# Kernel optimization log

Measured on AMD Instinct MI355X. Metric: run time of the kernel, lower is better.

The kernel has to match this reference:

```python
import jax, jax.numpy as jnp
import numpy as np

N_Q, N_X, N_Z = 1024, 512, 512
N_PER = N_Q + N_X + N_Z        # 2048 nodes per graph
B = 16                          # graphs per batch
DEG = 16                        # avg in/out degree
E_PER = N_PER * DEG
N = B * N_PER                   # 32768 total nodes
E = B * E_PER                   # 524288 total edges
HID, HEADS, L = 128, 4, 3
DH = HID // HEADS               # 32 per-head dim
EPS = 1e-5


def setup_inputs() -> dict:
    key = jax.random.key(0)
    ks = jax.random.split(key, 10)
    # one-hot node-type features (qubit / X-stab / Z-stab), tiled over batch
    sn = jnp.zeros((N_PER, 3), jnp.float32)
    sn = sn.at[:N_Q, 0].set(1.0).at[N_Q:N_Q + N_X, 1].set(1.0).at[N_Q + N_X:, 2].set(1.0)
    x = jnp.tile(sn, (B, 1))  # [N,3]
    # random sparse edges, graph-local then offset (mimics dense_to_sparse + Batch)
    src = jax.random.randint(ks[0], (B, E_PER), 0, N_PER)
    dst = jax.random.randint(ks[1], (B, E_PER), 0, N_PER)
    off = (jnp.arange(B) * N_PER)[:, None]
    edge_src = (src + off).reshape(-1).astype(jnp.int32)
    edge_dst = (dst + off).reshape(-1).astype(jnp.int32)
    seg = jnp.repeat(jnp.arange(B, dtype=jnp.int32), N_PER)  # graph id per node
    s = 0.05
    return dict(
        x=x, edge_src=edge_src, edge_dst=edge_dst, seg=seg,
        in_w=jax.random.normal(ks[2], (3, HID)) * s, in_b=jnp.zeros((HID,)),
        qw=jax.random.normal(ks[3], (L, HID, HID)) * s, qb=jnp.zeros((L, HID)),
        kw=jax.random.normal(ks[4], (L, HID, HID)) * s, kb=jnp.zeros((L, HID)),
        vw=jax.random.normal(ks[5], (L, HID, HID)) * s, vb=jnp.zeros((L, HID)),
        sw=jax.random.normal(ks[6], (L, HID, HID)) * s, sb=jnp.zeros((L, HID)),
        fw=jax.random.normal(ks[7], (L, HID, HID)) * s, fb=jnp.zeros((L, HID)),
        ln_g=jnp.ones((L, HID)), ln_b=jnp.zeros((L, HID)),
    )


def _layer_norm(h, g, b):
    mu = jnp.mean(h, axis=-1, keepdims=True)
    var = jnp.mean(jnp.square(h - mu), axis=-1, keepdims=True)
    return (h - mu) * jax.lax.rsqrt(var + EPS) * g + b


def reference(x, edge_src, edge_dst, seg, in_w, in_b, qw, qb, kw, kb, vw, vb,
              sw, sb, fw, fb, ln_g, ln_b):
    scale = 1.0 / jnp.sqrt(jnp.float32(DH))
    h = x @ in_w + in_b  # [N,HID]
    for i in range(L):
        h_res = h
        # TransformerConv: per-edge multi-head attention (softmax over in-neighbors)
        q = (h @ qw[i] + qb[i]).reshape(N, HEADS, DH)
        k = (h @ kw[i] + kb[i]).reshape(N, HEADS, DH)
        v = (h @ vw[i] + vb[i]).reshape(N, HEADS, DH)
        logits = jnp.einsum('ehd,ehd->eh', q[edge_dst], k[edge_src]) * scale  # [E,H]
        m = jax.ops.segment_max(logits, edge_dst, num_segments=N)             # [N,H]
        e = jnp.exp(logits - m[edge_dst])
        z = jax.ops.segment_sum(e, edge_dst, num_segments=N)                  # [N,H]
        alpha = e / z[edge_dst]
        agg = jax.ops.segment_sum(alpha[:, :, None] * v[edge_src], edge_dst,
                                  num_segments=N).reshape(N, HID)
        h = agg + h @ sw[i] + sb[i]        # root/skip linear (root_weight=True)
        # dropout is a no-op in eval mode
        h = h + jax.nn.relu(h @ fw[i] + fb[i])   # FFN residual
        h = h + h_res                            # outer residual
        h = jax.nn.relu(_layer_norm(h, ln_g[i], ln_b[i]))
    # global_mean_pool over graphs
    tot = jax.ops.segment_sum(h, seg, num_segments=B)                       # [B,HID]
    cnt = jax.ops.segment_sum(jnp.ones((N, 1), h.dtype), seg, num_segments=B)
    return tot / cnt
```

## Files before the change

### kernel.cpp

```cpp
#include <hip/hip_runtime.h>
#include <hip/hip_bf16.h>

#define N_TOT 32768
#define E_TOT 524288
#define HID 128
#define B_GR 16
#define NPER 2048
#define LAYERS 3
#define EPSLN 1e-5f
#define ELLW 64
#define SCALE 0.17677669529663687f

typedef float f4 __attribute__((ext_vector_type(4)));
typedef short bf16x8 __attribute__((ext_vector_type(8)));
typedef unsigned short u16x4 __attribute__((ext_vector_type(4)));

__device__ __forceinline__ unsigned short f2bf_rne(float x) {
    unsigned u = __float_as_uint(x);
    unsigned r = (u + 0x7FFFu + ((u >> 16) & 1u)) >> 16;
    return (unsigned short)r;
}

__device__ __forceinline__ float bf2f(unsigned short u) {
    return __uint_as_float(((unsigned)u) << 16);
}

__device__ __forceinline__ void unpack8(uint4 w, float* f) {
    f[0] = __uint_as_float(w.x << 16); f[1] = __uint_as_float(w.x & 0xFFFF0000u);
    f[2] = __uint_as_float(w.y << 16); f[3] = __uint_as_float(w.y & 0xFFFF0000u);
    f[4] = __uint_as_float(w.z << 16); f[5] = __uint_as_float(w.z & 0xFFFF0000u);
    f[6] = __uint_as_float(w.w << 16); f[7] = __uint_as_float(w.w & 0xFFFF0000u);
}

__global__ __launch_bounds__(256) void k_zp(const float* __restrict__ qw, const float* __restrict__ kw,
                                            const float* __restrict__ vw, const float* __restrict__ sw,
                                            const float* __restrict__ fw, unsigned short* __restrict__ wt,
                                            int* __restrict__ cursor, float* __restrict__ outz) {
    if (blockIdx.x < 960) {
        int mid = blockIdx.x >> 6;
        int within = (blockIdx.x & 63) * 256 + threadIdx.x;
        int l = mid / 5, t = mid % 5;
        const float* src = (t == 0 ? qw : t == 1 ? kw : t == 2 ? vw : t == 3 ? sw : fw) + l * HID * HID;
        int c = within >> 7;
        int kk = within & 127;
        int k = kk ^ ((c & 7) << 3);
        float sc = (t == 0) ? SCALE : 1.0f;
        wt[mid * HID * HID + c * HID + kk] = f2bf_rne(src[k * HID + c] * sc);
    } else if (blockIdx.x < 992) {
        int i = (blockIdx.x - 960) * 256 + threadIdx.x;
        reinterpret_cast<int4*>(cursor)[i] = int4{0, 0, 0, 0};
    } else {
        f4 z4 = {0.f, 0.f, 0.f, 0.f};
        reinterpret_cast<f4*>(outz)[threadIdx.x * 2] = z4;
        reinterpret_cast<f4*>(outz)[threadIdx.x * 2 + 1] = z4;
    }
}

__global__ __launch_bounds__(256) void k_scatter_ell(const int* __restrict__ src, const int* __restrict__ dst,
                                                     int* __restrict__ cursor, unsigned short* __restrict__ ell) {
    int e = blockIdx.x * 256 + threadIdx.x;
    if (e < E_TOT) {
        int d = dst[e];
        int pos = atomicAdd(&cursor[d], 1);
        if (pos < ELLW) ell[d * ELLW + pos] = (unsigned short)src[e];
    }
}

__device__ __forceinline__ void stage_A(const float* __restrict__ A, int r0,
                                        unsigned short (*A_lds)[HID], int tid) {
    #pragma unroll
    for (int p = 0; p < 8; ++p) {
        int idx = p * 256 + tid;
        int row = idx >> 5;
        int k0 = (idx & 31) * 4;
        f4 v = reinterpret_cast<const f4*>(A + (size_t)r0 * HID)[idx];
        u16x4 b = {f2bf_rne(v.x), f2bf_rne(v.y), f2bf_rne(v.z), f2bf_rne(v.w)};
        *reinterpret_cast<u16x4*>(&A_lds[row][k0 ^ ((row & 7) << 3)]) = b;
    }
}

#define GEMM_COMPUTE(acc, AL)                                                               \
    {                                                                                       \
        _Pragma("unroll")                                                                   \
        for (int ks = 0; ks < 4; ++ks) {                                                    \
            bf16x8 a0 = *reinterpret_cast<const bf16x8*>(                                   \
                &AL[wm * 32 + lr][(ks * 32 + lg * 8) ^ swz]);                               \
            bf16x8 a1 = *reinterpret_cast<const bf16x8*>(                                   \
                &AL[wm * 32 + 16 + lr][(ks * 32 + lg * 8) ^ swz]);                          \
            _Pragma("unroll")                                                               \
            for (int n = 0; n < 4; ++n) {                                                   \
                bf16x8 b = *reinterpret_cast<const bf16x8*>(                                \
                    &W_lds[wn * 64 + n * 16 + lr][(ks * 32 + lg * 8) ^ swz]);               \
                acc[0][n] = __builtin_amdgcn_mfma_f32_16x16x32_bf16(a0, b, acc[0][n], 0, 0, 0); \
                acc[1][n] = __builtin_amdgcn_mfma_f32_16x16x32_bf16(a1, b, acc[1][n], 0, 0, 0); \
            }                                                                               \
        }                                                                                   \
    }

#define QKV_EPILOGUE(ACC, T_IDX)                                                            \
    {                                                                                       \
        _Pragma("unroll")                                                                   \
        for (int n = 0; n < 4; ++n) {                                                       \
            int col = wn * 64 + n * 16 + lr;                                                \
            float bs = biases[T_IDX][col];                                                  \
            if (T_IDX == 0) bs *= SCALE;                                                    \
            unsigned short* outp = (T_IDX == 0) ? oq : okv + ((T_IDX == 2) ? 128 : 0);      \
            const size_t stride = (T_IDX == 0) ? HID : 256;                                 \
            _Pragma("unroll")                                                               \
            for (int m = 0; m < 2; ++m) {                                                   \
                _Pragma("unroll")                                                           \
                for (int r = 0; r < 4; ++r) {                                               \
                    int row = r0 + wm * 32 + m * 16 + lg * 4 + r;                           \
                    outp[(size_t)row * stride + col] = f2bf_rne(ACC[m][n][r] + bs);         \
                }                                                                           \
            }                                                                               \
        }                                                                                   \
    }

__global__ __launch_bounds__(256) void k_init_qkv(const float* __restrict__ x,
                                                  const float* __restrict__ in_w,
                                                  const float* __restrict__ in_b,
                                                  const unsigned short* __restrict__ wl,
                                                  const float* __restrict__ qb, const float* __restrict__ kb,
                                                  const float* __restrict__ vb,
                                                  float* __restrict__ h,
                                                  unsigned short* __restrict__ oq,
                                                  unsigned short* __restrict__ okv) {
    __shared__ unsigned short A_lds[64][HID];
    __shared__ unsigned short W_lds[HID][HID];
    int tid = threadIdx.x;
    int r0 = blockIdx.x * 64;
    int lane = tid & 63, w = tid >> 6;
    int wm = w >> 1, wn = w & 1;
    int lr = lane & 15, lg = lane >> 4;
    int swz = (lane & 7) << 3;

    #pragma unroll
    for (int p = 0; p < 8; ++p) {
        int idx = p * 256 + tid;
        int row = idx >> 5;
        int k0 = (idx & 31) * 4;
        int n = r0 + row;
        float x0 = x[n * 3 + 0], x1 = x[n * 3 + 1], x2 = x[n * 3 + 2];
        f4 o;
        #pragma unroll
        for (int i = 0; i < 4; ++i) {
            int c = k0 + i;
            o[i] = x0 * in_w[c] + x1 * in_w[HID + c] + x2 * in_w[2 * HID + c] + in_b[c];
        }
        reinterpret_cast<f4*>(h + (size_t)r0 * HID)[idx] = o;
        u16x4 b = {f2bf_rne(o[0]), f2bf_rne(o[1]), f2bf_rne(o[2]), f2bf_rne(o[3])};
        *reinterpret_cast<u16x4*>(&A_lds[row][k0 ^ ((row & 7) << 3)]) = b;
    }

    const float* biases[3] = {qb, kb, vb};
    #pragma unroll
    for (int t = 0; t < 3; ++t) {
        const unsigned short* Wp = wl + t * HID * HID;
        #pragma unroll
        for (int p = 0; p < 8; ++p) {
            int idx = p * 256 + tid;
            reinterpret_cast<f4*>(&W_lds[0][0])[idx] = reinterpret_cast<const f4*>(Wp)[idx];
        }
        __syncthreads();
        f4 acc[2][4];
        #pragma unroll
        for (int m = 0; m < 2; ++m)
            #pragma unroll
            for (int n = 0; n < 4; ++n) acc[m][n] = f4{0, 0, 0, 0};
        GEMM_COMPUTE(acc, A_lds);
        QKV_EPILOGUE(acc, t);
        __syncthreads();
    }
}

__global__ __launch_bounds__(256) void k_attn5(const unsigned short* __restrict__ qb16,
                                               const unsigned short* __restrict__ kv16,
                                               const int* __restrict__ deg,
                                               const unsigned short* __restrict__ ell,
                                               unsigned short* __restrict__ outagg) {
    int bid = blockIdx.x;
    int xcd = bid & 7;
    int chunk = bid >> 3;
    int g2 = xcd + 8 * (chunk >> 9);
    int nb = g2 * 512 + (chunk & 511);
    int n = nb * 4 + (threadIdx.x >> 6);

    int lane = threadIdx.x & 63;
    int g = lane >> 4, l = lane & 15;
    int dg = deg[n];
    if (dg > ELLW) dg = ELLW;
    const unsigned short* eb = ell + n * ELLW;

    float qf[8];
    {
        uint4 qw = *reinterpret_cast<const uint4*>(&qb16[(size_t)n * HID + l * 8]);
        unpack8(qw, qf);
    }

    float z = 0.f;
    float a[8] = {0, 0, 0, 0, 0, 0, 0, 0};
    int nit = (dg + 3) >> 2;
    if (nit > 0) {
        int j = g;
        bool val = j < dg;
        int sj = val ? (int)eb[j] : 0;
        const unsigned short* kv = kv16 + (size_t)sj * 256 + l * 8;
        uint4 kw = *reinterpret_cast<const uint4*>(kv);
        uint4 vw = *reinterpret_cast<const uint4*>(kv + 128);
        for (int it = 0; it < nit; ++it) {
            int jn = j + 4;
            bool valn = jn < dg;
            int sn = valn ? (int)eb[jn] : 0;
            const unsigned short* kvn = kv16 + (size_t)sn * 256 + l * 8;
            uint4 kwn = *reinterpret_cast<const uint4*>(kvn);
            uint4 vwn = *reinterpret_cast<const uint4*>(kvn + 128);
            float kf[8]; unpack8(kw, kf);
            float d = qf[0] * kf[0] + qf[1] * kf[1] + qf[2] * kf[2] + qf[3] * kf[3] +
                      qf[4] * kf[4] + qf[5] * kf[5] + qf[6] * kf[6] + qf[7] * kf[7];
            d += __shfl_xor(d, 1);
            d += __shfl_xor(d, 2);
            float p = val ? __expf(d) : 0.f;
            z += p;
            float vf[8]; unpack8(vw, vf);
            #pragma unroll
            for (int c = 0; c < 8; ++c) a[c] += p * vf[c];
            kw = kwn; vw = vwn; j = jn; val = valn;
        }
    }
    #pragma unroll
    for (int off = 16; off <= 32; off <<= 1) {
        z += __shfl_xor(z, off);
        #pragma unroll
        for (int c = 0; c < 8; ++c) a[c] += __shfl_xor(a[c], off);
    }
    if (g == 0) {
        float inv = (z > 0.f) ? 1.f / z : 0.f;
        uint4 o;
        o.x = (unsigned)f2bf_rne(a[0] * inv) | ((unsigned)f2bf_rne(a[1] * inv) << 16);
        o.y = (unsigned)f2bf_rne(a[2] * inv) | ((unsigned)f2bf_rne(a[3] * inv) << 16);
        o.z = (unsigned)f2bf_rne(a[4] * inv) | ((unsigned)f2bf_rne(a[5] * inv) << 16);
        o.w = (unsigned)f2bf_rne(a[6] * inv) | ((unsigned)f2bf_rne(a[7] * inv) << 16);
        *reinterpret_cast<uint4*>(&outagg[(size_t)n * HID + l * 8]) = o;
    }
}

template <bool QKV>
__global__ __launch_bounds__(256) void k_fused(const float* __restrict__ h,
                                               const unsigned short* __restrict__ wsf,
                                               const float* __restrict__ sb,
                                               const float* __restrict__ fb,
                                               const unsigned short* __restrict__ agg16,
                                               const float* __restrict__ gma,
                                               const float* __restrict__ beta,
                                               float* __restrict__ out,
                                               const unsigned short* __restrict__ wqkv,
                                               const float* __restrict__ qb2,
                                               const float* __restrict__ kb2,
                                               const float* __restrict__ vb2,
                                               unsigned short* __restrict__ oq,
                                               unsigned short* __restrict__ okv,
                                               float* __restrict__ pool_out) {
    __shared__ __align__(16) char smem[50432];
    unsigned short (*A_lds)[HID] = reinterpret_cast<unsigned short (*)[HID]>(smem);
    unsigned short (*W_lds)[HID] = reinterpret_cast<unsigned short (*)[HID]>(smem + 16384);
    float (*T)[133] = reinterpret_cast<float (*)[133]>(smem + 16384);

    int tid = threadIdx.x;
    int r0 = blockIdx.x * 64;
    int lane = tid & 63, w = tid >> 6;
    int wm = w >> 1, wn = w & 1;
    int lr = lane & 15, lg = lane >> 4;
    int swz = (lane & 7) << 3;

    stage_A(h, r0, A_lds, tid);
    #pragma unroll
    for (int p = 0; p < 8; ++p) {
        int idx = p * 256 + tid;
        reinterpret_cast<f4*>(&W_lds[0][0])[idx] = reinterpret_cast<const f4*>(wsf)[idx];
    }
    __syncthreads();
    f4 acc[2][4];
    #pragma unroll
    for (int m = 0; m < 2; ++m)
        #pragma unroll
        for (int n = 0; n < 4; ++n) acc[m][n] = f4{0, 0, 0, 0};
    GEMM_COMPUTE(acc, A_lds);
    __syncthreads();

    #pragma unroll
    for (int n = 0; n < 4; ++n) {
        int col = wn * 64 + n * 16 + lr;
        float bs = sb[col];
        #pragma unroll
        for (int m = 0; m < 2; ++m) {
            #pragma unroll
            for (int r = 0; r < 4; ++r) {
                int rl = wm * 32 + m * 16 + lg * 4 + r;
                float v = acc[m][n][r] + bs + bf2f(agg16[(size_t)(r0 + rl) * HID + col]);
                acc[m][n][r] = v;
                A_lds[rl][col ^ ((rl & 7) << 3)] = f2bf_rne(v);
            }
        }
    }
    #pragma unroll
    for (int p = 0; p < 8; ++p) {
        int idx = p * 256 + tid;
        reinterpret_cast<f4*>(&W_lds[0][0])[idx] = reinterpret_cast<const f4*>(wsf + HID * HID)[idx];
    }
    __syncthreads();
    f4 acc2[2][4];
    #pragma unroll
    for (int m = 0; m < 2; ++m)
        #pragma unroll
        for (int n = 0; n < 4; ++n) acc2[m][n] = f4{0, 0, 0, 0};
    GEMM_COMPUTE(acc2, A_lds);
    __syncthreads();

    #pragma unroll
    for (int n = 0; n < 4; ++n) {
        int col = wn * 64 + n * 16 + lr;
        float bs = fb[col];
        #pragma unroll
        for (int m = 0; m < 2; ++m) {
            #pragma unroll
            for (int r = 0; r < 4; ++r) {
                int rl = wm * 32 + m * 16 + lg * 4 + r;
                float t = acc[m][n][r] + fmaxf(acc2[m][n][r] + bs, 0.f) +
                          h[(size_t)(r0 + rl) * HID + col];
                T[rl][col] = t;
            }
        }
    }
    __syncthreads();

    int row = tid >> 2, qd = tid & 3;
    float s = 0.f, ss = 0.f;
    #pragma unroll 8
    for (int cc = 0; cc < 32; ++cc) {
        int c = (cc + qd * 8) & 31;
        float x = T[row][qd * 32 + c];
        s += x; ss += x * x;
    }
    s += __shfl_xor(s, 1);  s += __shfl_xor(s, 2);
    ss += __shfl_xor(ss, 1); ss += __shfl_xor(ss, 2);
    float mu = s * (1.f / 128.f);
    float var = ss * (1.f / 128.f) - mu * mu;
    float rsq = rsqrtf(fmaxf(var, 0.f) + EPSLN);
    int rswz = (row & 7) << 3;
    #pragma unroll
    for (int c4 = 0; c4 < 8; ++c4) {
        int cb = ((c4 + qd * 2) & 7) * 4;
        int col = qd * 32 + cb;
        f4 o;
        #pragma unroll
        for (int i = 0; i < 4; ++i) {
            float x = T[row][col + i];
            float y = (x - mu) * rsq * gma[col + i] + beta[col + i];
            o[i] = fmaxf(y, 0.f);
        }
        if (QKV) {
            *reinterpret_cast<f4*>(&out[(size_t)(r0 + row) * HID + col]) = o;
            u16x4 b = {f2bf_rne(o[0]), f2bf_rne(o[1]), f2bf_rne(o[2]), f2bf_rne(o[3])};
            *reinterpret_cast<u16x4*>(&A_lds[row][col ^ rswz]) = b;
        } else {
            #pragma unroll
            for (int i = 0; i < 4; ++i) T[row][col + i] = o[i];
        }
    }

    if (QKV) {
        __syncthreads();
        const float* biases[3] = {qb2, kb2, vb2};
        #pragma unroll
        for (int t = 0; t < 3; ++t) {
            const unsigned short* Wp = wqkv + t * HID * HID;
            #pragma unroll
            for (int p = 0; p < 8; ++p) {
                int idx = p * 256 + tid;
                reinterpret_cast<f4*>(&W_lds[0][0])[idx] = reinterpret_cast<const f4*>(Wp)[idx];
            }
            __syncthreads();
            f4 acc3[2][4];
            #pragma unroll
            for (int m = 0; m < 2; ++m)
                #pragma unroll
                for (int n = 0; n < 4; ++n) acc3[m][n] = f4{0, 0, 0, 0};
            GEMM_COMPUTE(acc3, A_lds);
            QKV_EPILOGUE(acc3, t);
            __syncthreads();
        }
    } else {
        __syncthreads();
        if (tid < HID) {
            float s2 = 0.f;
            #pragma unroll 8
            for (int r = 0; r < 64; ++r) s2 += T[r][tid];
            atomicAdd(&pool_out[(r0 >> 11) * HID + tid], s2 * (1.f / NPER));
        }
    }
}

extern "C" void kernel_launch(void* const* d_in, const int* in_sizes, int n_in,
                              void* d_out, int out_size, void* d_ws, size_t ws_size,
                              hipStream_t stream) {
    const float* x    = (const float*)d_in[0];
    const int*   esrc = (const int*)d_in[1];
    const int*   edst = (const int*)d_in[2];
    const float* in_w = (const float*)d_in[4];
    const float* in_b = (const float*)d_in[5];
    const float* qw   = (const float*)d_in[6];
    const float* qb   = (const float*)d_in[7];
    const float* kw   = (const float*)d_in[8];
    const float* kb   = (const float*)d_in[9];
    const float* vw   = (const float*)d_in[10];
    const float* vb   = (const float*)d_in[11];
    const float* sw   = (const float*)d_in[12];
    const float* sb   = (const float*)d_in[13];
    const float* fw   = (const float*)d_in[14];
    const float* fb   = (const float*)d_in[15];
    const float* ln_g = (const float*)d_in[16];
    const float* ln_b = (const float*)d_in[17];
    float* out = (float*)d_out;

    const size_t NH = (size_t)N_TOT * HID;
    float* h = (float*)d_ws;
    unsigned short* agg16 = (unsigned short*)(h + NH);
    unsigned short* qb16  = agg16 + NH;
    unsigned short* kv16  = qb16 + NH;
    unsigned short* wt    = kv16 + 2 * NH;
    int* cursor = (int*)(wt + 15 * HID * HID);
    unsigned short* ell = (unsigned short*)(cursor + N_TOT);

    k_zp<<<993, 256, 0, stream>>>(qw, kw, vw, sw, fw, wt, cursor, out);
    k_scatter_ell<<<E_TOT / 256, 256, 0, stream>>>(esrc, edst, cursor, ell);
    k_init_qkv<<<N_TOT / 64, 256, 0, stream>>>(x, in_w, in_b, wt, qb, kb, vb,
                                               h, qb16, kv16);

    for (int l = 0; l < LAYERS; ++l) {
        const unsigned short* wt_l = wt + (size_t)l * 5 * HID * HID;
        k_attn5<<<N_TOT / 4, 256, 0, stream>>>(qb16, kv16, cursor, ell, agg16);
        if (l + 1 < LAYERS) {
            const unsigned short* wt_n = wt + (size_t)(l + 1) * 5 * HID * HID;
            k_fused<true><<<N_TOT / 64, 256, 0, stream>>>(
                h, wt_l + 3 * HID * HID, sb + (size_t)l * HID, fb + (size_t)l * HID,
                agg16, ln_g + (size_t)l * HID, ln_b + (size_t)l * HID, h,
                wt_n, qb + (size_t)(l + 1) * HID, kb + (size_t)(l + 1) * HID,
                vb + (size_t)(l + 1) * HID, qb16, kv16, nullptr);
        } else {
            k_fused<false><<<N_TOT / 64, 256, 0, stream>>>(
                h, wt_l + 3 * HID * HID, sb + (size_t)l * HID, fb + (size_t)l * HID,
                agg16, ln_g + (size_t)l * HID, ln_b + (size_t)l * HID, h,
                nullptr, nullptr, nullptr, nullptr, nullptr, nullptr, out);
        }
    }
}
```

Measured before the change: 172.4 us.

## Store residual h as pre-swizzled bf16 and prefetch next weight tile into registers

The fp32 hidden state h becomes a bf16 buffer written in the swizzled LDS layout, and the aggregation output is written pre-swizzled too. The fused kernel can then copy both tiles straight into LDS with 16-byte loads and reuse the residual from LDS instead of a strided global fp32 read. The next weight matrix is also loaded into registers while the current GEMM runs, overlapping global loads with MFMA work. This halves h traffic but rounds the residual stream to bf16 across layers, which may lose accuracy, and uses more LDS and registers per block, which can lower occupancy.

```diff
diff --git a/kernel.cpp b/kernel.cpp
--- a/kernel.cpp
+++ b/kernel.cpp
@@ -66,19 +66,6 @@
     }
 }
 
-__device__ __forceinline__ void stage_A(const float* __restrict__ A, int r0,
-                                        unsigned short (*A_lds)[HID], int tid) {
-    #pragma unroll
-    for (int p = 0; p < 8; ++p) {
-        int idx = p * 256 + tid;
-        int row = idx >> 5;
-        int k0 = (idx & 31) * 4;
-        f4 v = reinterpret_cast<const f4*>(A + (size_t)r0 * HID)[idx];
-        u16x4 b = {f2bf_rne(v.x), f2bf_rne(v.y), f2bf_rne(v.z), f2bf_rne(v.w)};
-        *reinterpret_cast<u16x4*>(&A_lds[row][k0 ^ ((row & 7) << 3)]) = b;
-    }
-}
-
 #define GEMM_COMPUTE(acc, AL)                                                               \
     {                                                                                       \
         _Pragma("unroll")                                                                   \
@@ -95,6 +82,36 @@
                 acc[1][n] = __builtin_amdgcn_mfma_f32_16x16x32_bf16(a1, b, acc[1][n], 0, 0, 0); \
             }                                                                               \
         }                                                                                   \
+    }
+
+#define ZERO_ACC(acc)                                                        \
+    {                                                                        \
+        _Pragma("unroll")                                                    \
+        for (int m = 0; m < 2; ++m)                                          \
+            _Pragma("unroll")                                                \
+            for (int n = 0; n < 4; ++n) acc[m][n] = f4{0, 0, 0, 0};          \
+    }
+
+#define COPY_W(SRC)                                                          \
+    {                                                                        \
+        _Pragma("unroll")                                                    \
+        for (int p = 0; p < 8; ++p)                                          \
+            reinterpret_cast<uint4*>(&W_lds[0][0])[p * 256 + tid] =          \
+                reinterpret_cast<const uint4*>(SRC)[p * 256 + tid];          \
+    }
+
+#define LOAD_WREG(SRC)                                                       \
+    {                                                                        \
+        _Pragma("unroll")                                                    \
+        for (int p = 0; p < 8; ++p)                                          \
+            wreg[p] = reinterpret_cast<const uint4*>(SRC)[p * 256 + tid];    \
+    }
+
+#define WRITE_WREG()                                                         \
+    {                                                                        \
+        _Pragma("unroll")                                                    \
+        for (int p = 0; p < 8; ++p)                                          \
+            reinterpret_cast<uint4*>(&W_lds[0][0])[p * 256 + tid] = wreg[p]; \
     }
 
 #define QKV_EPILOGUE(ACC, T_IDX)                                                            \
@@ -123,7 +140,7 @@
                                                   const unsigned short* __restrict__ wl,
                                                   const float* __restrict__ qb, const float* __restrict__ kb,
                                                   const float* __restrict__ vb,
-                                                  float* __restrict__ h,
+                                                  unsigned short* __restrict__ h16,
                                                   unsigned short* __restrict__ oq,
                                                   unsigned short* __restrict__ okv) {
     __shared__ unsigned short A_lds[64][HID];
@@ -142,36 +159,39 @@
         int k0 = (idx & 31) * 4;
         int n = r0 + row;
         float x0 = x[n * 3 + 0], x1 = x[n * 3 + 1], x2 = x[n * 3 + 2];
-        f4 o;
+        u16x4 b;
         #pragma unroll
         for (int i = 0; i < 4; ++i) {
             int c = k0 + i;
-            o[i] = x0 * in_w[c] + x1 * in_w[HID + c] + x2 * in_w[2 * HID + c] + in_b[c];
-        }
-        reinterpret_cast<f4*>(h + (size_t)r0 * HID)[idx] = o;
-        u16x4 b = {f2bf_rne(o[0]), f2bf_rne(o[1]), f2bf_rne(o[2]), f2bf_rne(o[3])};
-        *reinterpret_cast<u16x4*>(&A_lds[row][k0 ^ ((row & 7) << 3)]) = b;
+            b[i] = f2bf_rne(x0 * in_w[c] + x1 * in_w[HID + c] + x2 * in_w[2 * HID + c] + in_b[c]);
+        }
+        int cs = k0 ^ ((row & 7) << 3);
+        *reinterpret_cast<u16x4*>(&A_lds[row][cs]) = b;
+        *reinterpret_cast<u16x4*>(&h16[(size_t)n * HID + cs]) = b;
     }
 
     const float* biases[3] = {qb, kb, vb};
-    #pragma unroll
-    for (int t = 0; t < 3; ++t) {
-        const unsigned short* Wp = wl + t * HID * HID;
-        #pragma unroll
-        for (int p = 0; p < 8; ++p) {
-            int idx = p * 256 + tid;
-            reinterpret_cast<f4*>(&W_lds[0][0])[idx] = reinterpret_cast<const f4*>(Wp)[idx];
-        }
-        __syncthreads();
-        f4 acc[2][4];
-        #pragma unroll
-        for (int m = 0; m < 2; ++m)
-            #pragma unroll
-            for (int n = 0; n < 4; ++n) acc[m][n] = f4{0, 0, 0, 0};
-        GEMM_COMPUTE(acc, A_lds);
-        QKV_EPILOGUE(acc, t);
-        __syncthreads();
-    }
+    uint4 wreg[8];
+    COPY_W(wl);
+    LOAD_WREG(wl + HID * HID);
+    __syncthreads();
+    f4 acc[2][4];
+    ZERO_ACC(acc);
+    GEMM_COMPUTE(acc, A_lds);
+    QKV_EPILOGUE(acc, 0);
+    __syncthreads();
+    WRITE_WREG();
+    LOAD_WREG(wl + 2 * HID * HID);
+    __syncthreads();
+    ZERO_ACC(acc);
+    GEMM_COMPUTE(acc, A_lds);
+    QKV_EPILOGUE(acc, 1);
+    __syncthreads();
+    WRITE_WREG();
+    __syncthreads();
+    ZERO_ACC(acc);
+    GEMM_COMPUTE(acc, A_lds);
+    QKV_EPILOGUE(acc, 2);
 }
 
 __global__ __launch_bounds__(256) void k_attn5(const unsigned short* __restrict__ qb16,
@@ -241,19 +261,19 @@
         o.y = (unsigned)f2bf_rne(a[2] * inv) | ((unsigned)f2bf_rne(a[3] * inv) << 16);
         o.z = (unsigned)f2bf_rne(a[4] * inv) | ((unsigned)f2bf_rne(a[5] * inv) << 16);
         o.w = (unsigned)f2bf_rne(a[6] * inv) | ((unsigned)f2bf_rne(a[7] * inv) << 16);
-        *reinterpret_cast<uint4*>(&outagg[(size_t)n * HID + l * 8]) = o;
+        *reinterpret_cast<uint4*>(&outagg[(size_t)n * HID + ((l ^ (n & 7)) * 8)]) = o;
     }
 }
 
 template <bool QKV>
-__global__ __launch_bounds__(256) void k_fused(const float* __restrict__ h,
+__global__ __launch_bounds__(256) void k_fused(const unsigned short* __restrict__ h16,
                                                const unsigned short* __restrict__ wsf,
                                                const float* __restrict__ sb,
                                                const float* __restrict__ fb,
                                                const unsigned short* __restrict__ agg16,
                                                const float* __restrict__ gma,
                                                const float* __restrict__ beta,
-                                               float* __restrict__ out,
+                                               unsigned short* __restrict__ out16,
                                                const unsigned short* __restrict__ wqkv,
                                                const float* __restrict__ qb2,
                                                const float* __restrict__ kb2,
@@ -261,9 +281,10 @@
                                                unsigned short* __restrict__ oq,
                                                unsigned short* __restrict__ okv,
                                                float* __restrict__ pool_out) {
-    __shared__ __align__(16) char smem[50432];
+    __shared__ __align__(16) char smem[65536];
     unsigned short (*A_lds)[HID] = reinterpret_cast<unsigned short (*)[HID]>(smem);
     unsigned short (*W_lds)[HID] = reinterpret_cast<unsigned short (*)[HID]>(smem + 16384);
+    unsigned short (*AG)[HID]    = reinterpret_cast<unsigned short (*)[HID]>(smem + 49152);
     float (*T)[133] = reinterpret_cast<float (*)[133]>(smem + 16384);
 
     int tid = threadIdx.x;
@@ -273,21 +294,26 @@
     int lr = lane & 15, lg = lane >> 4;
     int swz = (lane & 7) << 3;
 
-    stage_A(h, r0, A_lds, tid);
-    #pragma unroll
-    for (int p = 0; p < 8; ++p) {
-        int idx = p * 256 + tid;
-        reinterpret_cast<f4*>(&W_lds[0][0])[idx] = reinterpret_cast<const f4*>(wsf)[idx];
-    }
+    {
+        const uint4* hs = reinterpret_cast<const uint4*>(h16 + (size_t)r0 * HID);
+        const uint4* as = reinterpret_cast<const uint4*>(agg16 + (size_t)r0 * HID);
+        #pragma unroll
+        for (int p = 0; p < 4; ++p) {
+            reinterpret_cast<uint4*>(&A_lds[0][0])[p * 256 + tid] = hs[p * 256 + tid];
+            reinterpret_cast<uint4*>(&AG[0][0])[p * 256 + tid] = as[p * 256 + tid];
+        }
+    }
+    uint4 wreg[8];
+    COPY_W(wsf);
+    LOAD_WREG(wsf + HID * HID);
     __syncthreads();
     f4 acc[2][4];
-    #pragma unroll
-    for (int m = 0; m < 2; ++m)
-        #pragma unroll
-        for (int n = 0; n < 4; ++n) acc[m][n] = f4{0, 0, 0, 0};
+    ZERO_ACC(acc);
     GEMM_COMPUTE(acc, A_lds);
     __syncthreads();
-
+    WRITE_WREG();
+
+    unsigned short hres[2][4][4];
     #pragma unroll
     for (int n = 0; n < 4; ++n) {
         int col = wn * 64 + n * 16 + lr;
@@ -297,23 +323,17 @@
             #pragma unroll
             for (int r = 0; r < 4; ++r) {
                 int rl = wm * 32 + m * 16 + lg * 4 + r;
-                float v = acc[m][n][r] + bs + bf2f(agg16[(size_t)(r0 + rl) * HID + col]);
+                int cs = col ^ ((rl & 7) << 3);
+                hres[m][n][r] = A_lds[rl][cs];
+                float v = acc[m][n][r] + bs + bf2f(AG[rl][cs]);
                 acc[m][n][r] = v;
-                A_lds[rl][col ^ ((rl & 7) << 3)] = f2bf_rne(v);
+                A_lds[rl][cs] = f2bf_rne(v);
             }
         }
     }
-    #pragma unroll
-    for (int p = 0; p < 8; ++p) {
-        int idx = p * 256 + tid;
-        reinterpret_cast<f4*>(&W_lds[0][0])[idx] = reinterpret_cast<const f4*>(wsf + HID * HID)[idx];
-    }
     __syncthreads();
     f4 acc2[2][4];
-    #pragma unroll
-    for (int m = 0; m < 2; ++m)
-        #pragma unroll
-        for (int n = 0; n < 4; ++n) acc2[m][n] = f4{0, 0, 0, 0};
+    ZERO_ACC(acc2);
     GEMM_COMPUTE(acc2, A_lds);
     __syncthreads();
 
@@ -326,9 +346,7 @@
             #pragma unroll
             for (int r = 0; r < 4; ++r) {
                 int rl = wm * 32 + m * 16 + lg * 4 + r;
-                float t = acc[m][n][r] + fmaxf(acc2[m][n][r] + bs, 0.f) +
-                          h[(size_t)(r0 + rl) * HID + col];
-                T[rl][col] = t;
+                T[rl][col] = acc[m][n][r] + fmaxf(acc2[m][n][r] + bs, 0.f) + bf2f(hres[m][n][r]);
             }
         }
     }
@@ -360,9 +378,10 @@
             o[i] = fmaxf(y, 0.f);
         }
         if (QKV) {
-            *reinterpret_cast<f4*>(&out[(size_t)(r0 + row) * HID + col]) = o;
             u16x4 b = {f2bf_rne(o[0]), f2bf_rne(o[1]), f2bf_rne(o[2]), f2bf_rne(o[3])};
-            *reinterpret_cast<u16x4*>(&A_lds[row][col ^ rswz]) = b;
+            int cs = col ^ rswz;
+            *reinterpret_cast<u16x4*>(&A_lds[row][cs]) = b;
+            *reinterpret_cast<u16x4*>(&out16[(size_t)(r0 + row) * HID + cs]) = b;
         } else {
             #pragma unroll
             for (int i = 0; i < 4; ++i) T[row][col + i] = o[i];
@@ -370,26 +389,28 @@
     }
 
     if (QKV) {
-        __syncthreads();
         const float* biases[3] = {qb2, kb2, vb2};
-        #pragma unroll
-        for (int t = 0; t < 3; ++t) {
-            const unsigned short* Wp = wqkv + t * HID * HID;
-            #pragma unroll
-            for (int p = 0; p < 8; ++p) {
-                int idx = p * 256 + tid;
-                reinterpret_cast<f4*>(&W_lds[0][0])[idx] = reinterpret_cast<const f4*>(Wp)[idx];
-            }
-            __syncthreads();
-            f4 acc3[2][4];
-            #pragma unroll
-            for (int m = 0; m < 2; ++m)
-                #pragma unroll
-                for (int n = 0; n < 4; ++n) acc3[m][n] = f4{0, 0, 0, 0};
-            GEMM_COMPUTE(acc3, A_lds);
-            QKV_EPILOGUE(acc3, t);
-            __syncthreads();
-        }
+        __syncthreads();
+        COPY_W(wqkv);
+        LOAD_WREG(wqkv + HID * HID);
+        __syncthreads();
+        f4 acc3[2][4];
+        ZERO_ACC(acc3);
+        GEMM_COMPUTE(acc3, A_lds);
+        QKV_EPILOGUE(acc3, 0);
+        __syncthreads();
+        WRITE_WREG();
+        LOAD_WREG(wqkv + 2 * HID * HID);
+        __syncthreads();
+        ZERO_ACC(acc3);
+        GEMM_COMPUTE(acc3, A_lds);
+        QKV_EPILOGUE(acc3, 1);
+        __syncthreads();
+        WRITE_WREG();
+        __syncthreads();
+        ZERO_ACC(acc3);
+        GEMM_COMPUTE(acc3, A_lds);
+        QKV_EPILOGUE(acc3, 2);
     } else {
         __syncthreads();
         if (tid < HID) {
@@ -424,8 +445,8 @@
     float* out = (float*)d_out;
 
     const size_t NH = (size_t)N_TOT * HID;
-    float* h = (float*)d_ws;
-    unsigned short* agg16 = (unsigned short*)(h + NH);
+    unsigned short* h16   = (unsigned short*)d_ws;
+    unsigned short* agg16 = h16 + NH;
     unsigned short* qb16  = agg16 + NH;
     unsigned short* kv16  = qb16 + NH;
     unsigned short* wt    = kv16 + 2 * NH;
@@ -435,7 +456,7 @@
     k_zp<<<993, 256, 0, stream>>>(qw, kw, vw, sw, fw, wt, cursor, out);
     k_scatter_ell<<<E_TOT / 256, 256, 0, stream>>>(esrc, edst, cursor, ell);
     k_init_qkv<<<N_TOT / 64, 256, 0, stream>>>(x, in_w, in_b, wt, qb, kb, vb,
-                                               h, qb16, kv16);
+                                               h16, qb16, kv16);
 
     for (int l = 0; l < LAYERS; ++l) {
         const unsigned short* wt_l = wt + (size_t)l * 5 * HID * HID;
@@ -443,14 +464,14 @@
         if (l + 1 < LAYERS) {
             const unsigned short* wt_n = wt + (size_t)(l + 1) * 5 * HID * HID;
             k_fused<true><<<N_TOT / 64, 256, 0, stream>>>(
-                h, wt_l + 3 * HID * HID, sb + (size_t)l * HID, fb + (size_t)l * HID,
-                agg16, ln_g + (size_t)l * HID, ln_b + (size_t)l * HID, h,
+                h16, wt_l + 3 * HID * HID, sb + (size_t)l * HID, fb + (size_t)l * HID,
+                agg16, ln_g + (size_t)l * HID, ln_b + (size_t)l * HID, h16,
                 wt_n, qb + (size_t)(l + 1) * HID, kb + (size_t)(l + 1) * HID,
                 vb + (size_t)(l + 1) * HID, qb16, kv16, nullptr);
         } else {
             k_fused<false><<<N_TOT / 64, 256, 0, stream>>>(
-                h, wt_l + 3 * HID * HID, sb + (size_t)l * HID, fb + (size_t)l * HID,
-                agg16, ln_g + (size_t)l * HID, ln_b + (size_t)l * HID, h,
+                h16, wt_l + 3 * HID * HID, sb + (size_t)l * HID, fb + (size_t)l * HID,
+                agg16, ln_g + (size_t)l * HID, ln_b + (size_t)l * HID, nullptr,
                 nullptr, nullptr, nullptr, nullptr, nullptr, nullptr, out);
         }
     }
```

After: 198.7 us. +15.2%, slower.
